# Optimization experiments

Hardware: AMD Instinct MI355X
Metric: run time of the kernel (lower is better)

## Reference

```python
import jax, jax.numpy as jnp
import numpy as np

BS, NCAMS, CIN, H, W = 4, 1, 256, 56, 200
MID = 128
DCH = 112  # (58-2)/0.5 depth bins
GX, GY, GZ = 128, 128, 16  # voxel grid


def setup_inputs() -> dict:
    key = jax.random.key(0)
    ks = jax.random.split(key, 32)
    f32 = jnp.float32

    def n(k, shape, scale=0.05):
        return jax.random.normal(k, shape, f32) * scale

    inp = {
        'img_feat': jax.random.normal(ks[0], (BS, NCAMS, CIN, H, W), f32),
        'scaled_pixel_size': jax.random.uniform(ks[1], (BS * NCAMS, 1), f32) * 2.0 + 0.5,
        # normalized sampling coords, slightly beyond [-1,1] to exercise zero padding
        'grids': jax.random.uniform(ks[2], (NCAMS, BS, GX, GY, GZ, 3), f32) * 2.2 - 1.1,
        # reduce_conv: Conv2d(CIN->MID,3x3,bias) + BN(affine, eval=per-channel scale/shift)
        'rc_w': n(ks[3], (MID, CIN, 3, 3)),
        'rc_b': n(ks[4], (MID,)),
        'rc_s': 1.0 + n(ks[5], (MID,)),
        'rc_t': n(ks[6], (MID,)),
        # Mlp(1 -> MID -> MID)
        'fc1_w': n(ks[7], (MID, 1), 0.5),
        'fc1_b': n(ks[8], (MID,)),
        'fc2_w': n(ks[9], (MID, MID)),
        'fc2_b': n(ks[10], (MID,)),
        # SELayer 1x1 convs (act on [N,MID,1,1] -> plain linears)
        'se_rw': n(ks[11], (MID, MID)),
        'se_rb': n(ks[12], (MID,)),
        'se_ew': n(ks[13], (MID, MID)),
        'se_eb': n(ks[14], (MID,)),
        # 3 BasicBlocks: conv3x3(no bias)+BN+ReLU+conv3x3(no bias)+BN, residual, ReLU
        'bb_w1': n(ks[15], (3, MID, MID, 3, 3)),
        'bb_s1': 1.0 + n(ks[16], (3, MID)),
        'bb_t1': n(ks[17], (3, MID)),
        'bb_w2': n(ks[18], (3, MID, MID, 3, 3)),
        'bb_s2': 1.0 + n(ks[19], (3, MID)),
        'bb_t2': n(ks[20], (3, MID)),
        # depth_pred 1x1 conv MID -> DCH
        'dp_w': n(ks[21], (DCH, MID)),
        'dp_b': n(ks[22], (DCH,)),
    }
    return inp


def _conv2d(x, w):
    return jax.lax.conv_general_dilated(x, w, (1, 1), 'SAME',
                                        dimension_numbers=('NCHW', 'OIHW', 'NCHW'))


def _aff(x, s, t):
    return x * s[None, :, None, None] + t[None, :, None, None]


def grid_sample_3d(feat, grid):
    """Trilinear grid_sample, zeros padding, align_corners=False.
    feat: [N,C,D,H,W]; grid: [N,X,Y,Z,3] with (x,y,z) in [-1,1] indexing (W,H,D).
    Returns [N,C,X,Y,Z]."""
    N, C, D, Hh, Ww = feat.shape
    ix = (grid[..., 0] + 1.0) * (Ww * 0.5) - 0.5
    iy = (grid[..., 1] + 1.0) * (Hh * 0.5) - 0.5
    iz = (grid[..., 2] + 1.0) * (D * 0.5) - 0.5
    x0 = jnp.floor(ix); y0 = jnp.floor(iy); z0 = jnp.floor(iz)
    fx, fy, fz = ix - x0, iy - y0, iz - z0

    def one(f, x0, y0, z0, fx, fy, fz):
        out = jnp.zeros((C,) + x0.shape, f.dtype)
        x0i = x0.astype(jnp.int32); y0i = y0.astype(jnp.int32); z0i = z0.astype(jnp.int32)
        for dz in (0, 1):
            for dy in (0, 1):
                for dx in (0, 1):
                    xi = x0i + dx; yi = y0i + dy; zi = z0i + dz
                    wgt = ((fx if dx else 1.0 - fx) * (fy if dy else 1.0 - fy)
                           * (fz if dz else 1.0 - fz))
                    valid = ((xi >= 0) & (xi < Ww) & (yi >= 0) & (yi < Hh)
                             & (zi >= 0) & (zi < D))
                    v = f[:, jnp.clip(zi, 0, D - 1), jnp.clip(yi, 0, Hh - 1),
                          jnp.clip(xi, 0, Ww - 1)]
                    out = out + v * (wgt * valid)[None]
        return out

    return jax.vmap(one)(feat, x0, y0, z0, fx, fy, fz)


def reference(img_feat, scaled_pixel_size, grids, rc_w, rc_b, rc_s, rc_t,
              fc1_w, fc1_b, fc2_w, fc2_b, se_rw, se_rb, se_ew, se_eb,
              bb_w1, bb_s1, bb_t1, bb_w2, bb_s2, bb_t2, dp_w, dp_b):
    bs, n_cams, c, h, w = img_feat.shape
    x = img_feat.reshape(bs * n_cams, c, h, w)
    # DepthNet (infer_mode): reduce_conv
    x = jax.nn.relu(_aff(_conv2d(x, rc_w) + rc_b[None, :, None, None], rc_s, rc_t))
    # Mlp on scaled_pixel_size + SE gating
    hmid = jax.nn.relu(scaled_pixel_size @ fc1_w.T + fc1_b) @ fc2_w.T + fc2_b
    se = jax.nn.relu(hmid @ se_rw.T + se_rb) @ se_ew.T + se_eb
    x = x * jax.nn.sigmoid(se)[:, :, None, None]
    # 3 BasicBlocks
    for i in range(3):
        y = jax.nn.relu(_aff(_conv2d(x, bb_w1[i]), bb_s1[i], bb_t1[i]))
        y = _aff(_conv2d(y, bb_w2[i]), bb_s2[i], bb_t2[i])
        x = jax.nn.relu(x + y)
    # depth_pred 1x1 conv, softmax over depth bins
    depth_feat = jnp.einsum('nchw,dc->ndhw', x, dp_w) + dp_b[None, :, None, None]
    depth = jax.nn.softmax(depth_feat, axis=1)
    depth = depth.reshape(bs, n_cams, 1, DCH, h, w)
    # per-camera frustum -> voxel bilinear sampling
    all_voxel_features = []
    for i in range(n_cams):
        all_voxel_features.append(grid_sample_3d(depth[:, i], grids[i]))
    agg = all_voxel_features[0]  # n_cams == 1 path in original forward
    return agg  # [bs, 1, GX, GY, GZ]
```

## Files before the change

### kernel.cpp

```cpp
#include <hip/hip_runtime.h>
#include <math.h>

typedef _Float16 v8h __attribute__((ext_vector_type(8)));
typedef float v4f __attribute__((ext_vector_type(4)));
typedef float v16f __attribute__((ext_vector_type(16)));

__global__ void __launch_bounds__(256) prep_repack_kernel(
    const float* __restrict__ rc_w, const float* __restrict__ bb_w1,
    const float* __restrict__ bb_w2, const float* __restrict__ dp_w,
    const float* __restrict__ sps,
    const float* __restrict__ fc1_w, const float* __restrict__ fc1_b,
    const float* __restrict__ fc2_w, const float* __restrict__ fc2_b,
    const float* __restrict__ se_rw, const float* __restrict__ se_rb,
    const float* __restrict__ se_ew, const float* __restrict__ se_eb,
    _Float16* __restrict__ wrc, _Float16* __restrict__ wbb,
    _Float16* __restrict__ wdp, float* __restrict__ sig) {
  const int bx = blockIdx.x;
  const int tid = threadIdx.x;
  __shared__ float lds[4612];

  if (bx < 64) {
    const float* src = rc_w + (size_t)bx * 2 * 2304;
#pragma unroll
    for (int r = 0; r < 18; ++r) {
      int e = r * 256 + tid;
      int col = e / 2304;
      int rem = e - col * 2304;
      lds[col * 2305 + rem] = src[e];
    }
    __syncthreads();
#pragma unroll
    for (int ro = 0; ro < 3; ++ro) {
      int lidx = ro * 256 + tid;
      if (lidx < 576) {
        int col = lidx & 1;
        int r = lidx >> 1;
        int kh = r & 1;
        int ct = r >> 1;
        int tap = ct % 9, c16 = ct / 9;
        v8h o;
#pragma unroll
        for (int j = 0; j < 8; ++j)
          o[j] = (_Float16)lds[col * 2305 + (c16 * 16 + kh * 8 + j) * 9 + tap];
        *(v8h*)(wrc + ((size_t)r * 128 + bx * 2 + col) * 8) = o;
      }
    }
  } else if (bx < 256) {
    const int t = bx - 64;
    const int k = t >> 5, g = t & 31;
    const float* base = (k < 3) ? (bb_w1 + (size_t)k * 147456)
                                : (bb_w2 + (size_t)(k - 3) * 147456);
    const int cslot = (k < 3) ? (2 * k) : (2 * (k - 3) + 1);
    const float* src = base + (size_t)g * 4 * 1152;
#pragma unroll
    for (int r = 0; r < 18; ++r) {
      int e = r * 256 + tid;
      int col = e / 1152;
      int rem = e - col * 1152;
      lds[col * 1153 + rem] = src[e];
    }
    __syncthreads();
#pragma unroll
    for (int ro = 0; ro < 3; ++ro) {
      int lidx = ro * 256 + tid;
      if (lidx < 576) {
        int col = lidx & 3;
        int r = lidx >> 2;
        int kh = r & 1;
        int ct = r >> 1;
        int tap = ct % 9, c16 = ct / 9;
        v8h o;
#pragma unroll
        for (int j = 0; j < 8; ++j)
          o[j] = (_Float16)lds[col * 1153 + (c16 * 16 + kh * 8 + j) * 9 + tap];
        *(v8h*)(wbb + (size_t)cslot * 147456 + ((size_t)r * 128 + g * 4 + col) * 8) = o;
      }
    }
  } else if (bx < 263) {
    int s3 = (bx - 256) * 256 + tid;
    v8h o;
#pragma unroll
    for (int j = 0; j < 8; ++j) o[j] = (_Float16)dp_w[(size_t)s3 * 8 + j];
    *(v8h*)(wdp + (size_t)s3 * 8) = o;
  } else {
    const int j = tid;
    const bool on = j < 128;
    for (int b = 0; b < 4; ++b) {
      float h1 = 0.f;
      if (on) h1 = fmaxf(sps[b] * fc1_w[j] + fc1_b[j], 0.f);
      __syncthreads();
      if (on) lds[j] = h1;
      __syncthreads();
      float hm = 0.f;
      if (on) {
        hm = fc2_b[j];
        for (int k = 0; k < 128; ++k) hm += lds[k] * fc2_w[j * 128 + k];
      }
      __syncthreads();
      if (on) lds[j] = hm;
      __syncthreads();
      float t = 0.f;
      if (on) {
        t = se_rb[j];
        for (int k = 0; k < 128; ++k) t += lds[k] * se_rw[j * 128 + k];
        t = fmaxf(t, 0.f);
      }
      __syncthreads();
      if (on) lds[j] = t;
      __syncthreads();
      if (on) {
        float se = se_eb[j];
        for (int k = 0; k < 128; ++k) se += lds[k] * se_ew[j * 128 + k];
        sig[b * 128 + j] = 1.f / (1.f + expf(-se));
      }
      __syncthreads();
    }
  }
}

__global__ void __launch_bounds__(256) convert_kernel(
    const float* __restrict__ img, _Float16* __restrict__ act16) {
  const int i = blockIdx.x * 256 + threadIdx.x;
  const int cq = blockIdx.y;
  const int n = i / 11200;
  const int hw = i - n * 11200;
  const float* ip = img + (size_t)n * 2867200 + (size_t)(cq * 64) * 11200 + hw;
  float v[64];
#pragma unroll
  for (int k = 0; k < 64; ++k) v[k] = ip[(size_t)k * 11200];
  _Float16* op = act16 + (size_t)i * 256 + cq * 64;
#pragma unroll
  for (int g = 0; g < 8; ++g) {
    v8h o;
#pragma unroll
    for (int j = 0; j < 8; ++j) o[j] = (_Float16)v[g * 8 + j];
    *(v8h*)(op + g * 8) = o;
  }
}

template <int CIN, int MODE>
__global__ void __launch_bounds__(512, 4) conv3x3_kernel(
    const _Float16* __restrict__ act, const _Float16* __restrict__ wr,
    const _Float16* __restrict__ xprev, const float* __restrict__ bias,
    const float* __restrict__ sc, const float* __restrict__ tr,
    const float* __restrict__ sig_se, _Float16* __restrict__ out) {
  constexpr int NCH = CIN / 16;
  const int wt = blockIdx.x, ht = blockIdx.y;
  const int n = blockIdx.z >> 1, cg = blockIdx.z & 1;
  const int h0 = ht * 8, w0 = wt * 32;
  const int tid = threadIdx.x;
  const int wave = tid >> 6, lane = tid & 63;
  const int l31 = lane & 31, khalf = lane >> 5;
  const int wv = wave >> 1, kc = wave & 1;

  __shared__ alignas(16) _Float16 ldsA[2][2 * 340 * 8];
  __shared__ alignas(16) _Float16 ldsB[2][1152 * 8];

  size_t goffA[2];
  int loffA[2];
  bool exA[2], okA[2];
#pragma unroll
  for (int it = 0; it < 2; ++it) {
    int slot = it * 512 + tid;
    int pos = slot >> 1, part = slot & 1;
    int hh = pos / 34, ww = pos - hh * 34;
    int gh = h0 - 1 + hh, gw = w0 - 1 + ww;
    exA[it] = slot < 680;
    bool inimg = (unsigned)gh < 56u && (unsigned)gw < 200u;
    okA[it] = exA[it] && inimg;
    loffA[it] = (part * 340 + pos) * 8;
    int ghc = okA[it] ? gh : 0, gwc = okA[it] ? gw : 0;
    goffA[it] = (((size_t)n * 56 + ghc) * 200 + gwc) * CIN + part * 8;
  }
  size_t goffB[3];
  int loffB[3];
  bool exB[3];
#pragma unroll
  for (int it = 0; it < 3; ++it) {
    int slot = it * 512 + tid;
    exB[it] = slot < 1152;
    int s = exB[it] ? slot : 0;
    int tap = s >> 7, kh = (s >> 6) & 1, co = s & 63;
    goffB[it] = (((size_t)(tap * 2 + kh)) * 128 + cg * 64 + co) * 8;
    loffB[it] = s * 8;
  }

  const v8h zero8 = {(_Float16)0, (_Float16)0, (_Float16)0, (_Float16)0,
                     (_Float16)0, (_Float16)0, (_Float16)0, (_Float16)0};
  v8h preA0[2], preB0[3], preA1[2], preB1[3];
#pragma unroll
  for (int it = 0; it < 2; ++it) {
    preA0[it] = okA[it] ? *(const v8h*)(act + goffA[it]) : zero8;
    preA1[it] = okA[it] ? *(const v8h*)(act + goffA[it] + 16) : zero8;
  }
#pragma unroll
  for (int it = 0; it < 3; ++it) {
    preB0[it] = exB[it] ? *(const v8h*)(wr + goffB[it]) : zero8;
    preB1[it] = exB[it] ? *(const v8h*)(wr + goffB[it] + 18432) : zero8;
  }

  v16f acc[2];
#pragma unroll
  for (int mt = 0; mt < 2; ++mt)
#pragma unroll
    for (int r = 0; r < 16; ++r) acc[mt][r] = 0.f;

  auto compute = [&](const _Float16* aB, const _Float16* bB) {
#pragma unroll
    for (int dx = 0; dx < 3; ++dx) {
      v8h a[4];
#pragma unroll
      for (int r = 0; r < 4; ++r)
        a[r] = *(const v8h*)(aB + (khalf * 340 + (wv * 2 + r) * 34 + l31 + dx) * 8);
#pragma unroll
      for (int dy = 0; dy < 3; ++dy) {
        v8h bf = *(const v8h*)(bB + ((dy * 3 + dx) * 128 + khalf * 64 + kc * 32 + l31) * 8);
        acc[0] = __builtin_amdgcn_mfma_f32_32x32x16_f16(a[dy], bf, acc[0], 0, 0, 0);
        acc[1] = __builtin_amdgcn_mfma_f32_32x32x16_f16(a[dy + 1], bf, acc[1], 0, 0, 0);
      }
    }
  };

#pragma unroll 1
  for (int c = 0; c < NCH; c += 2) {
#pragma unroll
    for (int it = 0; it < 2; ++it)
      if (exA[it]) *(v8h*)(&ldsA[0][0] + loffA[it]) = preA0[it];
#pragma unroll
    for (int it = 0; it < 3; ++it)
      if (exB[it]) *(v8h*)(&ldsB[0][0] + loffB[it]) = preB0[it];
    if (c + 2 < NCH) {
#pragma unroll
      for (int it = 0; it < 2; ++it)
        preA0[it] = okA[it] ? *(const v8h*)(act + goffA[it] + (size_t)(c + 2) * 16) : zero8;
#pragma unroll
      for (int it = 0; it < 3; ++it)
        preB0[it] = exB[it] ? *(const v8h*)(wr + goffB[it] + (size_t)(c + 2) * 18432) : zero8;
    }
    __syncthreads();
    compute(&ldsA[0][0], &ldsB[0][0]);

#pragma unroll
    for (int it = 0; it < 2; ++it)
      if (exA[it]) *(v8h*)(&ldsA[1][0] + loffA[it]) = preA1[it];
#pragma unroll
    for (int it = 0; it < 3; ++it)
      if (exB[it]) *(v8h*)(&ldsB[1][0] + loffB[it]) = preB1[it];
    if (c + 3 < NCH) {
#pragma unroll
      for (int it = 0; it < 2; ++it)
        preA1[it] = okA[it] ? *(const v8h*)(act + goffA[it] + (size_t)(c + 3) * 16) : zero8;
#pragma unroll
      for (int it = 0; it < 3; ++it)
        preB1[it] = exB[it] ? *(const v8h*)(wr + goffB[it] + (size_t)(c + 3) * 18432) : zero8;
    }
    __syncthreads();
    compute(&ldsA[1][0], &ldsB[1][0]);
  }

#pragma unroll
  for (int mt = 0; mt < 2; ++mt) {
    const int h = h0 + wv * 2 + mt;
    const int cc = cg * 64 + kc * 32 + l31;
    const float s = sc[cc], t = tr[cc];
    float bb = 0.f, sg = 1.f;
    if constexpr (MODE == 0) {
      bb = bias[cc];
      sg = sig_se[n * 128 + cc];
    }
#pragma unroll
    for (int r = 0; r < 16; ++r) {
      const int m = (r & 3) + 8 * (r >> 2) + 4 * khalf;
      const int w = w0 + m;
      if (w < 200) {
        float v = acc[mt][r];
        size_t oidx = (((size_t)n * 56 + h) * 200 + w) * 128 + cc;
        if constexpr (MODE == 0) v = fmaxf((v + bb) * s + t, 0.f) * sg;
        if constexpr (MODE == 1) v = fmaxf(v * s + t, 0.f);
        if constexpr (MODE == 2) v = fmaxf((float)xprev[oidx] + v * s + t, 0.f);
        out[oidx] = (_Float16)v;
      }
    }
  }
}

__global__ void __launch_bounds__(256) depth_proj_softmax_kernel(
    const _Float16* __restrict__ x, const _Float16* __restrict__ wdp,
    const float* __restrict__ dp_b, _Float16* __restrict__ depth) {
  const int wave = threadIdx.x >> 6, lane = threadIdx.x & 63;
  const int q = lane >> 4, l16 = lane & 15;
  const int pos0 = blockIdx.x * 64 + wave * 16;

  v4f acc[7];
#pragma unroll
  for (int nt = 0; nt < 7; ++nt) {
    float bv = dp_b[nt * 16 + l16];
    acc[nt] = {bv, bv, bv, bv};
  }
#pragma unroll
  for (int c0 = 0; c0 < 128; c0 += 32) {
    v8h a = *(const v8h*)(x + (size_t)(pos0 + l16) * 128 + c0 + q * 8);
#pragma unroll
    for (int nt = 0; nt < 7; ++nt) {
      v8h b = *(const v8h*)(wdp + (size_t)(nt * 16 + l16) * 128 + c0 + q * 8);
      acc[nt] = __builtin_amdgcn_mfma_f32_16x16x32_f16(a, b, acc[nt], 0, 0, 0);
    }
  }
  float m[4];
#pragma unroll
  for (int r = 0; r < 4; ++r) {
    m[r] = acc[0][r];
#pragma unroll
    for (int nt = 1; nt < 7; ++nt) m[r] = fmaxf(m[r], acc[nt][r]);
  }
#pragma unroll
  for (int off = 1; off < 16; off <<= 1)
#pragma unroll
    for (int r = 0; r < 4; ++r) m[r] = fmaxf(m[r], __shfl_xor(m[r], off));
  float s[4] = {0.f, 0.f, 0.f, 0.f};
#pragma unroll
  for (int nt = 0; nt < 7; ++nt)
#pragma unroll
    for (int r = 0; r < 4; ++r) {
      float e = expf(acc[nt][r] - m[r]);
      acc[nt][r] = e;
      s[r] += e;
    }
#pragma unroll
  for (int off = 1; off < 16; off <<= 1)
#pragma unroll
    for (int r = 0; r < 4; ++r) s[r] += __shfl_xor(s[r], off);
#pragma unroll
  for (int r = 0; r < 4; ++r) {
    const float inv = 1.f / s[r];
    const size_t p = pos0 + q * 4 + r;
#pragma unroll
    for (int nt = 0; nt < 7; ++nt)
      depth[p * 112 + nt * 16 + l16] = (_Float16)(acc[nt][r] * inv);
  }
}

__global__ void __launch_bounds__(256) gridsample_kernel(
    const float* __restrict__ grids, const _Float16* __restrict__ depth,
    float* __restrict__ out) {
  const int i = blockIdx.x * 256 + threadIdx.x;
  const int n = i >> 18;
  const float gx = grids[(size_t)i * 3];
  const float gy = grids[(size_t)i * 3 + 1];
  const float gz = grids[(size_t)i * 3 + 2];
  const float ix = (gx + 1.f) * 100.f - 0.5f;
  const float iy = (gy + 1.f) * 28.f - 0.5f;
  const float iz = (gz + 1.f) * 56.f - 0.5f;
  const float xf = floorf(ix), yf = floorf(iy), zf = floorf(iz);
  const int x0 = (int)xf, y0 = (int)yf, z0 = (int)zf;
  const float fx = ix - xf, fy = iy - yf, fz = iz - zf;
  const bool zv0 = (unsigned)z0 < 112u;
  const bool zv1 = (unsigned)(z0 + 1) < 112u;
  const float wz0 = 1.f - fz, wz1 = fz;
  float acc = 0.f;
#pragma unroll
  for (int dy = 0; dy < 2; ++dy) {
    const int yi = y0 + dy;
    const float wy = dy ? fy : 1.f - fy;
#pragma unroll
    for (int dx = 0; dx < 2; ++dx) {
      const int xi = x0 + dx;
      const float wx = dx ? fx : 1.f - fx;
      if ((unsigned)xi < 200u && (unsigned)yi < 56u) {
        const _Float16* bp = depth + ((size_t)n * 11200 + yi * 200 + xi) * 112;
        float v0 = zv0 ? (float)bp[z0] : 0.f;
        float v1 = zv1 ? (float)bp[z0 + 1] : 0.f;
        acc += (wx * wy) * (wz0 * v0 + wz1 * v1);
      }
    }
  }
  out[i] = acc;
}

extern "C" void kernel_launch(void* const* d_in, const int* in_sizes, int n_in,
                              void* d_out, int out_size, void* d_ws, size_t ws_size,
                              hipStream_t stream) {
  (void)in_sizes; (void)n_in; (void)out_size; (void)ws_size;
  const float* img = (const float*)d_in[0];
  const float* sps = (const float*)d_in[1];
  const float* grids = (const float*)d_in[2];
  const float* rc_w = (const float*)d_in[3];
  const float* rc_b = (const float*)d_in[4];
  const float* rc_s = (const float*)d_in[5];
  const float* rc_t = (const float*)d_in[6];
  const float* fc1_w = (const float*)d_in[7];
  const float* fc1_b = (const float*)d_in[8];
  const float* fc2_w = (const float*)d_in[9];
  const float* fc2_b = (const float*)d_in[10];
  const float* se_rw = (const float*)d_in[11];
  const float* se_rb = (const float*)d_in[12];
  const float* se_ew = (const float*)d_in[13];
  const float* se_eb = (const float*)d_in[14];
  const float* bb_w1 = (const float*)d_in[15];
  const float* bb_s1 = (const float*)d_in[16];
  const float* bb_t1 = (const float*)d_in[17];
  const float* bb_w2 = (const float*)d_in[18];
  const float* bb_s2 = (const float*)d_in[19];
  const float* bb_t2 = (const float*)d_in[20];
  const float* dp_w = (const float*)d_in[21];
  const float* dp_b = (const float*)d_in[22];
  float* outp = (float*)d_out;

  char* ws = (char*)d_ws;
  _Float16* act16 = (_Float16*)(ws + 0);
  _Float16* depth16 = (_Float16*)(ws + 0);
  _Float16* xa = (_Float16*)(ws + 23068672);
  _Float16* xb = (_Float16*)(ws + 23068672 + 11534336);
  _Float16* yb = (_Float16*)(ws + 23068672 + 2 * 11534336);
  _Float16* wrc = (_Float16*)(ws + 57671680);
  _Float16* wdp = (_Float16*)(ws + 57671680 + 589824);
  _Float16* wbb = (_Float16*)(ws + 58327040);
  float* sig = (float*)(ws + 58327040 + 1769472);

  prep_repack_kernel<<<dim3(264), 256, 0, stream>>>(
      rc_w, bb_w1, bb_w2, dp_w, sps, fc1_w, fc1_b, fc2_w, fc2_b, se_rw, se_rb,
      se_ew, se_eb, wrc, wbb, wdp, sig);
  convert_kernel<<<dim3(175, 4), 256, 0, stream>>>(img, act16);

  dim3 cgrid(7, 7, 8);
  conv3x3_kernel<256, 0><<<cgrid, 512, 0, stream>>>(act16, wrc, nullptr, rc_b, rc_s,
                                                    rc_t, sig, xa);
  _Float16* xcur = xa;
  _Float16* xnxt = xb;
  for (int i = 0; i < 3; ++i) {
    conv3x3_kernel<128, 1><<<cgrid, 512, 0, stream>>>(
        xcur, wbb + (size_t)(2 * i) * 147456, nullptr, nullptr, bb_s1 + i * 128,
        bb_t1 + i * 128, nullptr, yb);
    conv3x3_kernel<128, 2><<<cgrid, 512, 0, stream>>>(
        yb, wbb + (size_t)(2 * i + 1) * 147456, xcur, nullptr, bb_s2 + i * 128,
        bb_t2 + i * 128, nullptr, xnxt);
    _Float16* t = xcur;
    xcur = xnxt;
    xnxt = t;
  }

  depth_proj_softmax_kernel<<<dim3(700), 256, 0, stream>>>(xcur, wdp, dp_b, depth16);
  gridsample_kernel<<<dim3(4096), 256, 0, stream>>>(grids, depth16, outp);
}
```

Baseline: 417.6 us.

## Halve conv3x3 tile height, use 256-thread blocks with swizzled 1D grid

```diff
diff --git a/kernel.cpp b/kernel.cpp
--- a/kernel.cpp
+++ b/kernel.cpp
@@ -139,21 +139,25 @@
 }
 
 template <int CIN, int MODE>
-__global__ void __launch_bounds__(512, 4) conv3x3_kernel(
+__global__ void __launch_bounds__(256, 3) conv3x3_kernel(
     const _Float16* __restrict__ act, const _Float16* __restrict__ wr,
     const _Float16* __restrict__ xprev, const float* __restrict__ bias,
     const float* __restrict__ sc, const float* __restrict__ tr,
     const float* __restrict__ sig_se, _Float16* __restrict__ out) {
   constexpr int NCH = CIN / 16;
-  const int wt = blockIdx.x, ht = blockIdx.y;
-  const int n = blockIdx.z >> 1, cg = blockIdx.z & 1;
-  const int h0 = ht * 8, w0 = wt * 32;
+  const int fid = blockIdx.x;
+  const int swz = (fid & 7) * 98 + (fid >> 3);
+  const int zz = swz / 98;
+  const int tt = swz - zz * 98;
+  const int ht = tt / 7, wt = tt - ht * 7;
+  const int n = zz >> 1, cg = zz & 1;
+  const int h0 = ht * 4, w0 = wt * 32;
   const int tid = threadIdx.x;
   const int wave = tid >> 6, lane = tid & 63;
   const int l31 = lane & 31, khalf = lane >> 5;
   const int wv = wave >> 1, kc = wave & 1;
 
-  __shared__ alignas(16) _Float16 ldsA[2][2 * 340 * 8];
+  __shared__ alignas(16) _Float16 ldsA[2][2 * 204 * 8];
   __shared__ alignas(16) _Float16 ldsB[2][1152 * 8];
 
   size_t goffA[2];
@@ -161,23 +165,23 @@
   bool exA[2], okA[2];
 #pragma unroll
   for (int it = 0; it < 2; ++it) {
-    int slot = it * 512 + tid;
+    int slot = it * 256 + tid;
     int pos = slot >> 1, part = slot & 1;
     int hh = pos / 34, ww = pos - hh * 34;
     int gh = h0 - 1 + hh, gw = w0 - 1 + ww;
-    exA[it] = slot < 680;
+    exA[it] = slot < 408;
     bool inimg = (unsigned)gh < 56u && (unsigned)gw < 200u;
     okA[it] = exA[it] && inimg;
-    loffA[it] = (part * 340 + pos) * 8;
+    loffA[it] = (part * 204 + pos) * 8;
     int ghc = okA[it] ? gh : 0, gwc = okA[it] ? gw : 0;
     goffA[it] = (((size_t)n * 56 + ghc) * 200 + gwc) * CIN + part * 8;
   }
-  size_t goffB[3];
-  int loffB[3];
-  bool exB[3];
-#pragma unroll
-  for (int it = 0; it < 3; ++it) {
-    int slot = it * 512 + tid;
+  size_t goffB[5];
+  int loffB[5];
+  bool exB[5];
+#pragma unroll
+  for (int it = 0; it < 5; ++it) {
+    int slot = it * 256 + tid;
     exB[it] = slot < 1152;
     int s = exB[it] ? slot : 0;
     int tap = s >> 7, kh = (s >> 6) & 1, co = s & 63;
@@ -187,17 +191,11 @@
 
   const v8h zero8 = {(_Float16)0, (_Float16)0, (_Float16)0, (_Float16)0,
                      (_Float16)0, (_Float16)0, (_Float16)0, (_Float16)0};
-  v8h preA0[2], preB0[3], preA1[2], preB1[3];
-#pragma unroll
-  for (int it = 0; it < 2; ++it) {
-    preA0[it] = okA[it] ? *(const v8h*)(act + goffA[it]) : zero8;
-    preA1[it] = okA[it] ? *(const v8h*)(act + goffA[it] + 16) : zero8;
-  }
-#pragma unroll
-  for (int it = 0; it < 3; ++it) {
-    preB0[it] = exB[it] ? *(const v8h*)(wr + goffB[it]) : zero8;
-    preB1[it] = exB[it] ? *(const v8h*)(wr + goffB[it] + 18432) : zero8;
-  }
+  v8h preA[2], preB[5];
+#pragma unroll
+  for (int it = 0; it < 2; ++it) preA[it] = okA[it] ? *(const v8h*)(act + goffA[it]) : zero8;
+#pragma unroll
+  for (int it = 0; it < 5; ++it) preB[it] = exB[it] ? *(const v8h*)(wr + goffB[it]) : zero8;
 
   v16f acc[2];
 #pragma unroll
@@ -205,13 +203,31 @@
 #pragma unroll
     for (int r = 0; r < 16; ++r) acc[mt][r] = 0.f;
 
-  auto compute = [&](const _Float16* aB, const _Float16* bB) {
+#pragma unroll 1
+  for (int c = 0; c < NCH; ++c) {
+    _Float16* aB = &ldsA[c & 1][0];
+    _Float16* bB = &ldsB[c & 1][0];
+#pragma unroll
+    for (int it = 0; it < 2; ++it)
+      if (exA[it]) *(v8h*)(aB + loffA[it]) = preA[it];
+#pragma unroll
+    for (int it = 0; it < 5; ++it)
+      if (exB[it]) *(v8h*)(bB + loffB[it]) = preB[it];
+    __syncthreads();
+    if (c + 1 < NCH) {
+#pragma unroll
+      for (int it = 0; it < 2; ++it)
+        preA[it] = okA[it] ? *(const v8h*)(act + goffA[it] + (size_t)(c + 1) * 16) : zero8;
+#pragma unroll
+      for (int it = 0; it < 5; ++it)
+        preB[it] = exB[it] ? *(const v8h*)(wr + goffB[it] + (size_t)(c + 1) * 18432) : zero8;
+    }
 #pragma unroll
     for (int dx = 0; dx < 3; ++dx) {
       v8h a[4];
 #pragma unroll
       for (int r = 0; r < 4; ++r)
-        a[r] = *(const v8h*)(aB + (khalf * 340 + (wv * 2 + r) * 34 + l31 + dx) * 8);
+        a[r] = *(const v8h*)(aB + (khalf * 204 + (wv * 2 + r) * 34 + l31 + dx) * 8);
 #pragma unroll
       for (int dy = 0; dy < 3; ++dy) {
         v8h bf = *(const v8h*)(bB + ((dy * 3 + dx) * 128 + khalf * 64 + kc * 32 + l31) * 8);
@@ -219,43 +235,7 @@
         acc[1] = __builtin_amdgcn_mfma_f32_32x32x16_f16(a[dy + 1], bf, acc[1], 0, 0, 0);
       }
     }
-  };
-
-#pragma unroll 1
-  for (int c = 0; c < NCH; c += 2) {
-#pragma unroll
-    for (int it = 0; it < 2; ++it)
-      if (exA[it]) *(v8h*)(&ldsA[0][0] + loffA[it]) = preA0[it];
-#pragma unroll
-    for (int it = 0; it < 3; ++it)
-      if (exB[it]) *(v8h*)(&ldsB[0][0] + loffB[it]) = preB0[it];
-    if (c + 2 < NCH) {
-#pragma unroll
-      for (int it = 0; it < 2; ++it)
-        preA0[it] = okA[it] ? *(const v8h*)(act + goffA[it] + (size_t)(c + 2) * 16) : zero8;
-#pragma unroll
-      for (int it = 0; it < 3; ++it)
-        preB0[it] = exB[it] ? *(const v8h*)(wr + goffB[it] + (size_t)(c + 2) * 18432) : zero8;
-    }
     __syncthreads();
-    compute(&ldsA[0][0], &ldsB[0][0]);
-
-#pragma unroll
-    for (int it = 0; it < 2; ++it)
-      if (exA[it]) *(v8h*)(&ldsA[1][0] + loffA[it]) = preA1[it];
-#pragma unroll
-    for (int it = 0; it < 3; ++it)
-      if (exB[it]) *(v8h*)(&ldsB[1][0] + loffB[it]) = preB1[it];
-    if (c + 3 < NCH) {
-#pragma unroll
-      for (int it = 0; it < 2; ++it)
-        preA1[it] = okA[it] ? *(const v8h*)(act + goffA[it] + (size_t)(c + 3) * 16) : zero8;
-#pragma unroll
-      for (int it = 0; it < 3; ++it)
-        preB1[it] = exB[it] ? *(const v8h*)(wr + goffB[it] + (size_t)(c + 3) * 18432) : zero8;
-    }
-    __syncthreads();
-    compute(&ldsA[1][0], &ldsB[1][0]);
   }
 
 #pragma unroll
@@ -422,16 +402,16 @@
       se_ew, se_eb, wrc, wbb, wdp, sig);
   convert_kernel<<<dim3(175, 4), 256, 0, stream>>>(img, act16);
 
-  dim3 cgrid(7, 7, 8);
-  conv3x3_kernel<256, 0><<<cgrid, 512, 0, stream>>>(act16, wrc, nullptr, rc_b, rc_s,
+  dim3 cgrid(784);
+  conv3x3_kernel<256, 0><<<cgrid, 256, 0, stream>>>(act16, wrc, nullptr, rc_b, rc_s,
                                                     rc_t, sig, xa);
   _Float16* xcur = xa;
   _Float16* xnxt = xb;
   for (int i = 0; i < 3; ++i) {
-    conv3x3_kernel<128, 1><<<cgrid, 512, 0, stream>>>(
+    conv3x3_kernel<128, 1><<<cgrid, 256, 0, stream>>>(
         xcur, wbb + (size_t)(2 * i) * 147456, nullptr, nullptr, bb_s1 + i * 128,
         bb_t1 + i * 128, nullptr, yb);
-    conv3x3_kernel<128, 2><<<cgrid, 512, 0, stream>>>(
+    conv3x3_kernel<128, 2><<<cgrid, 256, 0, stream>>>(
         yb, wbb + (size_t)(2 * i + 1) * 147456, xcur, nullptr, bb_s2 + i * 128,
         bb_t2 + i * 128, nullptr, xnxt);
     _Float16* t = xcur;
```

Result: slower. 447.3 us (+7.1%).
